# Optimization experiments

Measured on AMD Instinct MI355X. Metric: run time of the kernel, lower is better.

## Reference

```python
import jax, jax.numpy as jnp
import numpy as np
from jax import lax

B, C_IN, C_MID, C_OUT, H, W = 8, 256, 128, 256, 128, 128
DN = ('NCHW', 'OIHW', 'NCHW')


def conv_bn(x, w, scale, shift, pad, relu):
    # conv (bias=False) + eval-mode BatchNorm folded to per-channel scale/shift
    y = lax.conv_general_dilated(x, w, (1, 1), [(pad, pad), (pad, pad)],
                                 dimension_numbers=DN)
    y = y * scale[None, :, None, None] + shift[None, :, None, None]
    return jax.nn.relu(y) if relu else y


def setup_inputs() -> dict:
    key = jax.random.key(0)
    ks = jax.random.split(key, 20)
    d = {"x": jax.random.normal(ks[0], (B, C_IN, H, W), dtype=jnp.float32)}
    f = 0.05  # weight scale
    def wparams(i, cout, cin, k):
        kk = jax.random.split(ks[i], 3)
        return (jax.random.normal(kk[0], (cout, cin, k, k), jnp.float32) * f,
                1.0 + 0.1 * jax.random.normal(kk[1], (cout,), jnp.float32),
                0.1 * jax.random.normal(kk[2], (cout,), jnp.float32))
    d["w_l"], d["s_l"], d["o_l"] = wparams(1, C_MID, C_IN, 3)
    d["w_r"], d["s_r"], d["o_r"] = wparams(2, C_MID, C_IN, 3)
    d["w_t"], d["s_t"], d["o_t"] = wparams(3, C_MID, C_IN, 3)
    d["w_b"], d["s_b"], d["o_b"] = wparams(4, C_MID, C_IN, 3)
    d["w2"], d["s2"], d["o2"] = wparams(5, C_OUT, C_MID, 3)
    d["w1"], d["s1"], d["o1"] = wparams(6, C_IN, C_IN, 1)
    return d


def reference(x, w_l, s_l, o_l, w_r, s_r, o_r, w_t, s_t, o_t,
              w_b, s_b, o_b, w2, s2, o2, w1, s1, o1):
    # four directional branches: conv+bn+relu then corner pooling (cummax scan)
    xl = lax.cummax(conv_bn(x, w_l, s_l, o_l, 1, True), axis=3, reverse=True)  # left: max over w'>=w
    xr = lax.cummax(conv_bn(x, w_r, s_r, o_r, 1, True), axis=3)                # right: max over w'<=w
    xt = lax.cummax(conv_bn(x, w_t, s_t, o_t, 1, True), axis=2, reverse=True)  # top: max over h'>=h
    xb = lax.cummax(conv_bn(x, w_b, s_b, o_b, 1, True), axis=2)                # bottom: max over h'<=h
    x1 = conv_bn(xl + xr + xb + xt, w2, s2, o2, 1, False)  # 3x3 conv+bn, no relu
    x2 = conv_bn(x, w1, s1, o1, 0, False)                  # 1x1 conv+bn skip, no relu
    return jax.nn.relu(x1 + x2)
```

## Files before the change

### kernel.cpp

```cpp
#include <hip/hip_runtime.h>

#define NEG_INF (-3.402823466e+38f)

typedef __bf16 bf16x8 __attribute__((ext_vector_type(8)));
typedef float  f32x16 __attribute__((ext_vector_type(16)));

__device__ __forceinline__ unsigned short f2bf(float f){
    unsigned u = __builtin_bit_cast(unsigned, f);
    u += 0x7fffu + ((u >> 16) & 1u);
    return (unsigned short)(u >> 16);
}
__device__ __forceinline__ float bf2f(unsigned short h){
    unsigned u = ((unsigned)h) << 16;
    return __builtin_bit_cast(float, u);
}

#if defined(__has_builtin)
#if __has_builtin(__builtin_amdgcn_global_load_lds)
#define ASYNC_CP 1
#endif
#endif

__device__ __forceinline__ void gl_lds(const unsigned short* g, unsigned short* lbase, int lane) {
#ifdef ASYNC_CP
    __builtin_amdgcn_global_load_lds(
        (const __attribute__((address_space(1))) unsigned int*)g,
        (__attribute__((address_space(3))) unsigned int*)lbase, 16, 0, 0);
#else
    *(uint4*)(lbase + (size_t)lane * 8) = *(const uint4*)g;
#endif
}

__global__ void __launch_bounds__(256)
k_xpose(const float* __restrict__ x, unsigned short* __restrict__ xh)
{
    __shared__ float tile[64 * 129];
    const int t = threadIdx.x;
    const int ci0 = blockIdx.x * 64, h = blockIdx.y, b = blockIdx.z;
    const float4* src = (const float4*)x;
#pragma unroll
    for (int i = 0; i < 8; ++i) {
        int idx = t + i * 256;
        int ci = idx >> 5, w4 = idx & 31;
        float4 v = src[((b * 256 + ci0 + ci) * 128 + h) * 32 + w4];
        tile[ci * 129 + w4 * 4 + 0] = v.x;
        tile[ci * 129 + w4 * 4 + 1] = v.y;
        tile[ci * 129 + w4 * 4 + 2] = v.z;
        tile[ci * 129 + w4 * 4 + 3] = v.w;
    }
    __syncthreads();
    unsigned* dst = (unsigned*)xh;
#pragma unroll
    for (int i = 0; i < 16; ++i) {
        int idx = t + i * 256;
        int w = idx >> 5, cp = idx & 31;
        float lo = tile[(cp * 2 + 0) * 129 + w];
        float hi = tile[(cp * 2 + 1) * 129 + w];
        dst[((b * 128 + h) * 128 + w) * 128 + (ci0 >> 1) + cp] =
            (unsigned)f2bf(lo) | ((unsigned)f2bf(hi) << 16);
    }
}

__global__ void __launch_bounds__(256)
k_wpack(const float* __restrict__ wl, const float* __restrict__ sl, const float* __restrict__ ol,
        const float* __restrict__ wr, const float* __restrict__ sr, const float* __restrict__ orr,
        const float* __restrict__ wt, const float* __restrict__ st, const float* __restrict__ ot,
        const float* __restrict__ wb, const float* __restrict__ sb, const float* __restrict__ ob,
        const float* __restrict__ w2, const float* __restrict__ s2, const float* __restrict__ o2,
        const float* __restrict__ w1, const float* __restrict__ s1, const float* __restrict__ o1,
        unsigned short* __restrict__ wpkBR, unsigned short* __restrict__ wpk2,
        unsigned short* __restrict__ wpk1, float* __restrict__ shF, float* __restrict__ obF)
{
    int i = blockIdx.x * 256 + threadIdx.x;
    if (i < 1179648) {
        int br = i / 294912, r = i % 294912;
        int c = r / 2304, r2 = r % 2304, ci = r2 / 9, k9 = r2 % 9;
        const float* wp = br == 0 ? wl : br == 1 ? wr : br == 2 ? wt : wb;
        const float* sp = br == 0 ? sl : br == 1 ? sr : br == 2 ? st : sb;
        float v = wp[r] * sp[c];
        int p = (c >> 4) * 64 + br * 16 + (c & 15);
        wpkBR[(((((ci >> 4) * 9 + k9) * 2 + ((ci >> 3) & 1)) * 512 + p) * 8) + (ci & 7)] = f2bf(v);
    } else if (i < 1474560) {
        int j = i - 1179648;
        int c = j / 1152, r2 = j % 1152, ci = r2 / 9, k9 = r2 % 9;
        wpk2[(((((ci >> 4) * 9 + k9) * 2 + ((ci >> 3) & 1)) * 256 + c) * 8) + (ci & 7)] = f2bf(w2[j] * s2[c]);
    } else if (i < 1540096) {
        int j = i - 1474560;
        int c = j >> 8, ci = j & 255;
        wpk1[((((ci >> 4) * 2 + ((ci >> 3) & 1)) * 256 + c) * 8) + (ci & 7)] = f2bf(w1[j] * s1[c]);
    } else if (i < 1540608) {
        int p = i - 1540096;
        int br = (p >> 4) & 3, c = (p >> 6) * 16 + (p & 15);
        const float* op = br == 0 ? ol : br == 1 ? orr : br == 2 ? ot : ob;
        shF[p] = op[c];
    } else if (i < 1540864) {
        int c = i - 1540608;
        obF[c] = o2[c] + o1[c];
    }
}

#define XIN_SH 12672
#define WBUF_SH 9216
__global__ void __launch_bounds__(256, 2)
k_brconv(const unsigned short* __restrict__ xh, const unsigned short* __restrict__ wpkBR,
         const float* __restrict__ shF, unsigned short* __restrict__ sbuf2,
         unsigned short* __restrict__ ytbT, unsigned short* __restrict__ ytbB)
{
    __shared__ __align__(16) unsigned short smem[2 * XIN_SH + WBUF_SH + 128];
    unsigned short* xinA = smem;
    unsigned short* xinB = smem + XIN_SH;
    unsigned short* wbuf = smem + 2 * XIN_SH;
    float* shs = (float*)(smem + 2 * XIN_SH + WBUF_SH);

    const int t = threadIdx.x;
    const int lin = (int)blockIdx.x + ((int)blockIdx.y << 3) + ((int)blockIdx.z << 8);
    const int swz = (lin & 7) * 256 + (lin >> 3);
    const int bx = swz & 7, h0 = ((swz >> 3) & 31) << 2, b = swz >> 8;
    const int wv = t >> 6, lane = t & 63;
    const int lo5 = lane & 31, hi1 = lane >> 5;
    const int hi32 = lane & 32;

    if (t < 64) shs[t] = shF[bx * 64 + t];
    for (int idx = t; idx < 3168; idx += 256)
        *(uint4*)(smem + idx * 8) = make_uint4(0, 0, 0, 0);

    f32x16 acc[2][4];
#pragma unroll
    for (int ct = 0; ct < 2; ++ct)
#pragma unroll
        for (int nb = 0; nb < 4; ++nb)
#pragma unroll
            for (int i = 0; i < 16; ++i) acc[ct][nb][i] = 0.f;

    __syncthreads();

    for (int s = wv; s < 24; s += 4) {
        int r = s >> 2, khi = (s >> 1) & 1, half = s & 1;
        int ih = h0 - 1 + r;
        if (ih >= 0 && ih < 128)
            gl_lds(xh + (((size_t)(b * 128 + ih) * 128 + half * 64 + lane) * 256) + khi * 8,
                   xinA + ((r * 2 + khi) * 132 + 1 + half * 64) * 8, lane);
    }
    for (int s = wv; s < 18; s += 4)
        gl_lds(wpkBR + ((size_t)s * 512 + bx * 64 + lane) * 8, wbuf + s * 512, lane);
    __syncthreads();

    uint4 wr0 = make_uint4(0, 0, 0, 0), wr1 = wr0, wr2 = wr0, wr3 = wr0, wr4 = wr0;
    unsigned short* xcur = xinA;
    unsigned short* xnxt = xinB;

    for (int cb = 0; cb < 16; ++cb) {
        if (cb < 15) {
            const int nc = cb + 1;
            for (int s = wv; s < 24; s += 4) {
                int r = s >> 2, khi = (s >> 1) & 1, half = s & 1;
                int ih = h0 - 1 + r;
                if (ih >= 0 && ih < 128)
                    gl_lds(xh + (((size_t)(b * 128 + ih) * 128 + half * 64 + lane) * 256) + nc * 16 + khi * 8,
                           xnxt + ((r * 2 + khi) * 132 + 1 + half * 64) * 8, lane);
            }
            wr0 = *(const uint4*)(wpkBR + ((size_t)(nc * 18 + wv) * 512 + bx * 64 + lane) * 8);
            wr1 = *(const uint4*)(wpkBR + ((size_t)(nc * 18 + wv + 4) * 512 + bx * 64 + lane) * 8);
            wr2 = *(const uint4*)(wpkBR + ((size_t)(nc * 18 + wv + 8) * 512 + bx * 64 + lane) * 8);
            wr3 = *(const uint4*)(wpkBR + ((size_t)(nc * 18 + wv + 12) * 512 + bx * 64 + lane) * 8);
            if (wv < 2)
                wr4 = *(const uint4*)(wpkBR + ((size_t)(nc * 18 + wv + 16) * 512 + bx * 64 + lane) * 8);
        }
#pragma unroll
        for (int k9 = 0; k9 < 9; ++k9) {
            const int kh = k9 / 3, kw = k9 % 3;
            bf16x8 a0 = *(const bf16x8*)(wbuf + ((k9 * 2 + hi1) * 64 + lo5) * 8);
            bf16x8 a1 = *(const bf16x8*)(wbuf + ((k9 * 2 + hi1) * 64 + 32 + lo5) * 8);
#pragma unroll
            for (int nb = 0; nb < 4; ++nb) {
                bf16x8 bf = *(const bf16x8*)(xcur + (((wv + kh) * 2 + hi1) * 132 + nb * 32 + lo5 + kw) * 8);
                acc[0][nb] = __builtin_amdgcn_mfma_f32_32x32x16_bf16(a0, bf, acc[0][nb], 0, 0, 0);
                acc[1][nb] = __builtin_amdgcn_mfma_f32_32x32x16_bf16(a1, bf, acc[1][nb], 0, 0, 0);
            }
        }
        __syncthreads();
        if (cb < 15) {
            *(uint4*)(wbuf + (wv) * 512 + lane * 8) = wr0;
            *(uint4*)(wbuf + (wv + 4) * 512 + lane * 8) = wr1;
            *(uint4*)(wbuf + (wv + 8) * 512 + lane * 8) = wr2;
            *(uint4*)(wbuf + (wv + 12) * 512 + lane * 8) = wr3;
            if (wv < 2)
                *(uint4*)(wbuf + (wv + 16) * 512 + lane * 8) = wr4;
            __syncthreads();
            unsigned short* tp = xcur; xcur = xnxt; xnxt = tp;
        }
    }

    unsigned short* pbw = smem + wv * 3072;
    const int hg = h0 + wv;

#pragma unroll
    for (int r = 0; r < 8; ++r) {
        const int m = (r & 3) + 8 * (r >> 2) + 4 * hi1;
        const float shv = shs[m];
        float carry = NEG_INF;
#pragma unroll
        for (int nn = 3; nn >= 0; --nn) {
            float a = fmaxf(acc[0][nn][r] + shv, 0.f);
#pragma unroll
            for (int d = 1; d < 32; d <<= 1) {
                float o = __shfl_down(a, d);
                if (lo5 < 32 - d) a = fmaxf(a, o);
            }
            a = fmaxf(a, carry);
            carry = __shfl(a, hi32);
            acc[0][nn][r] = a;
        }
    }
#pragma unroll
    for (int r = 8; r < 16; ++r) {
        const int m = 16 + (r & 3) + 8 * ((r >> 2) & 1) + 4 * hi1;
        const float shv = shs[m];
        float carry = NEG_INF;
#pragma unroll
        for (int nn = 0; nn < 4; ++nn) {
            float a = fmaxf(acc[0][nn][r] + shv, 0.f);
#pragma unroll
            for (int d = 1; d < 32; d <<= 1) {
                float o = __shfl_up(a, d);
                if (lo5 >= d) a = fmaxf(a, o);
            }
            a = fmaxf(a, carry);
            carry = __shfl(a, hi32 | 31);
            acc[0][nn][r] = a;
        }
    }
#pragma unroll
    for (int r = 0; r < 8; ++r) {
        const int c16 = (r & 3) + 8 * (r >> 2) + 4 * hi1;
#pragma unroll
        for (int nn = 0; nn < 4; ++nn)
            pbw[(nn * 32 + lo5) * 24 + c16] = f2bf(acc[0][nn][r] + acc[0][nn][r + 8]);
    }
    {
        unsigned short* gdst = sbuf2 + ((size_t)(b * 128 + hg) * 128) * 128 + bx * 16;
#pragma unroll
        for (int i = 0; i < 4; ++i) {
            int idx = lane + i * 64;
            int w = idx >> 1, part = idx & 1;
            *(uint4*)(gdst + (size_t)w * 128 + part * 8) = *(const uint4*)(pbw + w * 24 + part * 8);
        }
    }
#pragma unroll
    for (int r = 0; r < 8; ++r) {
        const int c16 = (r & 3) + 8 * (r >> 2) + 4 * hi1;
        const float shv = shs[32 + c16];
#pragma unroll
        for (int nn = 0; nn < 4; ++nn)
            pbw[(nn * 32 + lo5) * 24 + c16] = f2bf(fmaxf(acc[1][nn][r] + shv, 0.f));
    }
    {
        unsigned short* gdst = ytbT + ((size_t)(b * 128 + hg) * 128) * 128 + bx * 16;
#pragma unroll
        for (int i = 0; i < 4; ++i) {
            int idx = lane + i * 64;
            int w = idx >> 1, part = idx & 1;
            *(uint4*)(gdst + (size_t)w * 128 + part * 8) = *(const uint4*)(pbw + w * 24 + part * 8);
        }
    }
#pragma unroll
    for (int r = 8; r < 16; ++r) {
        const int c16 = (r & 3) + 8 * ((r >> 2) & 1) + 4 * hi1;
        const float shv = shs[48 + c16];
#pragma unroll
        for (int nn = 0; nn < 4; ++nn)
            pbw[(nn * 32 + lo5) * 24 + c16] = f2bf(fmaxf(acc[1][nn][r] + shv, 0.f));
    }
    {
        unsigned short* gdst = ytbB + ((size_t)(b * 128 + hg) * 128) * 128 + bx * 16;
#pragma unroll
        for (int i = 0; i < 4; ++i) {
            int idx = lane + i * 64;
            int w = idx >> 1, part = idx & 1;
            *(uint4*)(gdst + (size_t)w * 128 + part * 8) = *(const uint4*)(pbw + w * 24 + part * 8);
        }
    }
}

__global__ void __launch_bounds__(256)
k_colscan2(const unsigned short* __restrict__ ytbT, const unsigned short* __restrict__ ytbB,
           unsigned short* __restrict__ sbuf2)
{
    __shared__ float tile[8][8][33];
    const int t = threadIdx.x;
    const int w0 = blockIdx.x * 8, c0 = blockIdx.y * 32, b = blockIdx.z;
    const int sc = t & 31, sw = t >> 5;
    const int rh = t >> 5, r5 = t & 31;
    const int rw = r5 >> 2, rcq = r5 & 3;

    {
        float cum = NEG_INF;
        for (int step = 0; step < 16; ++step) {
            int h0 = 120 - step * 8;
            for (int q = 0; q < 8; ++q) {
                int hh = 7 - q;
                int hg = h0 + hh;
                float v = bf2f(ytbT[((b * 128 + hg) * 128 + (w0 + sw)) * 128 + c0 + sc]);
                cum = fmaxf(cum, v);
                tile[hh][sw][sc] = cum;
            }
            __syncthreads();
            {
                int hg = h0 + rh;
                unsigned short* p = sbuf2 + ((b * 128 + hg) * 128 + w0 + rw) * 128 + c0 + rcq * 8;
                uint4 u = *(uint4*)p;
                unsigned short* us = (unsigned short*)&u;
#pragma unroll
                for (int j = 0; j < 8; ++j)
                    us[j] = f2bf(bf2f(us[j]) + tile[rh][rw][rcq * 8 + j]);
                *(uint4*)p = u;
            }
            __syncthreads();
        }
    }
    {
        float cum = NEG_INF;
        for (int step = 0; step < 16; ++step) {
            int h0 = step * 8;
            for (int q = 0; q < 8; ++q) {
                int hh = q;
                int hg = h0 + hh;
                float v = bf2f(ytbB[((b * 128 + hg) * 128 + (w0 + sw)) * 128 + c0 + sc]);
                cum = fmaxf(cum, v);
                tile[hh][sw][sc] = cum;
            }
            __syncthreads();
            {
                int hg = h0 + rh;
                unsigned short* p = sbuf2 + ((b * 128 + hg) * 128 + w0 + rw) * 128 + c0 + rcq * 8;
                uint4 u = *(uint4*)p;
                unsigned short* us = (unsigned short*)&u;
#pragma unroll
                for (int j = 0; j < 8; ++j)
                    us[j] = f2bf(bf2f(us[j]) + tile[rh][rw][rcq * 8 + j]);
                *(uint4*)p = u;
            }
            __syncthreads();
        }
    }
}

__global__ void __launch_bounds__(256, 2)
k_final(const unsigned short* __restrict__ sbuf2, const unsigned short* __restrict__ xh,
        const unsigned short* __restrict__ wpk2, const unsigned short* __restrict__ wpk1,
        const float* __restrict__ obF, float* __restrict__ out)
{
    __shared__ __align__(16) unsigned short smem[2 * XIN_SH + WBUF_SH + 128];
    unsigned short* xinA = smem;
    unsigned short* xinB = smem + XIN_SH;
    unsigned short* wbuf = smem + 2 * XIN_SH;
    float* obs = (float*)(smem + 2 * XIN_SH + WBUF_SH);

    const int t = threadIdx.x;
    const int lin = (int)blockIdx.x + ((int)blockIdx.y << 2) + ((int)blockIdx.z << 7);
    const int swz = (lin & 7) * 128 + (lin >> 3);
    const int bx = swz & 3, h0 = ((swz >> 2) & 31) << 2, b = swz >> 7;
    const int wv = t >> 6, lane = t & 63;
    const int lo5 = lane & 31, hi1 = lane >> 5;

    if (t < 64) obs[t] = obF[bx * 64 + t];
    for (int idx = t; idx < 3168; idx += 256)
        *(uint4*)(smem + idx * 8) = make_uint4(0, 0, 0, 0);

    f32x16 acc[2][4];
#pragma unroll
    for (int ct = 0; ct < 2; ++ct)
#pragma unroll
        for (int nb = 0; nb < 4; ++nb)
#pragma unroll
            for (int i = 0; i < 16; ++i) acc[ct][nb][i] = 0.f;

    __syncthreads();

    for (int s = wv; s < 24; s += 4) {
        int r = s >> 2, khi = (s >> 1) & 1, half = s & 1;
        int ih = h0 - 1 + r;
        if (ih >= 0 && ih < 128)
            gl_lds(sbuf2 + (((size_t)(b * 128 + ih) * 128 + half * 64 + lane) * 128) + khi * 8,
                   xinA + ((r * 2 + khi) * 132 + 1 + half * 64) * 8, lane);
    }
    for (int s = wv; s < 18; s += 4)
        gl_lds(wpk2 + ((size_t)s * 256 + bx * 64 + lane) * 8, wbuf + s * 512, lane);
    __syncthreads();

    uint4 wr0 = make_uint4(0, 0, 0, 0), wr1 = wr0, wr2 = wr0, wr3 = wr0, wr4 = wr0;
    unsigned short* xcur = xinA;
    unsigned short* xnxt = xinB;

    for (int cb = 0; cb < 8; ++cb) {
        if (cb < 7) {
            const int nc = cb + 1;
            for (int s = wv; s < 24; s += 4) {
                int r = s >> 2, khi = (s >> 1) & 1, half = s & 1;
                int ih = h0 - 1 + r;
                if (ih >= 0 && ih < 128)
                    gl_lds(sbuf2 + (((size_t)(b * 128 + ih) * 128 + half * 64 + lane) * 128) + nc * 16 + khi * 8,
                           xnxt + ((r * 2 + khi) * 132 + 1 + half * 64) * 8, lane);
            }
            wr0 = *(const uint4*)(wpk2 + ((size_t)(nc * 18 + wv) * 256 + bx * 64 + lane) * 8);
            wr1 = *(const uint4*)(wpk2 + ((size_t)(nc * 18 + wv + 4) * 256 + bx * 64 + lane) * 8);
            wr2 = *(const uint4*)(wpk2 + ((size_t)(nc * 18 + wv + 8) * 256 + bx * 64 + lane) * 8);
            wr3 = *(const uint4*)(wpk2 + ((size_t)(nc * 18 + wv + 12) * 256 + bx * 64 + lane) * 8);
            if (wv < 2)
                wr4 = *(const uint4*)(wpk2 + ((size_t)(nc * 18 + wv + 16) * 256 + bx * 64 + lane) * 8);
        }
#pragma unroll
        for (int k9 = 0; k9 < 9; ++k9) {
            const int kh = k9 / 3, kw = k9 % 3;
            bf16x8 a0 = *(const bf16x8*)(wbuf + ((k9 * 2 + hi1) * 64 + lo5) * 8);
            bf16x8 a1 = *(const bf16x8*)(wbuf + ((k9 * 2 + hi1) * 64 + 32 + lo5) * 8);
#pragma unroll
            for (int nb = 0; nb < 4; ++nb) {
                bf16x8 bf = *(const bf16x8*)(xcur + (((wv + kh) * 2 + hi1) * 132 + nb * 32 + lo5 + kw) * 8);
                acc[0][nb] = __builtin_amdgcn_mfma_f32_32x32x16_bf16(a0, bf, acc[0][nb], 0, 0, 0);
                acc[1][nb] = __builtin_amdgcn_mfma_f32_32x32x16_bf16(a1, bf, acc[1][nb], 0, 0, 0);
            }
        }
        __syncthreads();
        if (cb < 7) {
            *(uint4*)(wbuf + (wv) * 512 + lane * 8) = wr0;
            *(uint4*)(wbuf + (wv + 4) * 512 + lane * 8) = wr1;
            *(uint4*)(wbuf + (wv + 8) * 512 + lane * 8) = wr2;
            *(uint4*)(wbuf + (wv + 12) * 512 + lane * 8) = wr3;
            if (wv < 2)
                *(uint4*)(wbuf + (wv + 16) * 512 + lane * 8) = wr4;
            __syncthreads();
            unsigned short* tp = xcur; xcur = xnxt; xnxt = tp;
        }
    }

    {
        const unsigned short* xrow = xh + ((size_t)(b * 128 + h0 + wv) * 128) * 256 + hi1 * 8;
        const unsigned short* w1p  = wpk1 + ((size_t)hi1 * 256 + bx * 64) * 8;
#pragma unroll 4
        for (int cb = 0; cb < 16; ++cb) {
            bf16x8 a0 = *(const bf16x8*)(w1p + ((size_t)cb * 512 + lo5) * 8);
            bf16x8 a1 = *(const bf16x8*)(w1p + ((size_t)cb * 512 + 32 + lo5) * 8);
#pragma unroll
            for (int nb = 0; nb < 4; ++nb) {
                bf16x8 bf = *(const bf16x8*)(xrow + (size_t)(nb * 32 + lo5) * 256 + cb * 16);
                acc[0][nb] = __builtin_amdgcn_mfma_f32_32x32x16_bf16(a0, bf, acc[0][nb], 0, 0, 0);
                acc[1][nb] = __builtin_amdgcn_mfma_f32_32x32x16_bf16(a1, bf, acc[1][nb], 0, 0, 0);
            }
        }
    }

    const int hg = h0 + wv;
#pragma unroll
    for (int ct = 0; ct < 2; ++ct)
#pragma unroll
        for (int r = 0; r < 16; ++r) {
            const int m = ct * 32 + (r & 3) + 8 * (r >> 2) + 4 * hi1;
            const float bias = obs[m];
#pragma unroll
            for (int nb = 0; nb < 4; ++nb)
                out[((size_t)(b * 256 + bx * 64 + m) * 128 + hg) * 128 + nb * 32 + lo5] =
                    fmaxf(acc[ct][nb][r] + bias, 0.f);
        }
}

extern "C" void kernel_launch(void* const* d_in, const int* in_sizes, int n_in,
                              void* d_out, int out_size, void* d_ws, size_t ws_size,
                              hipStream_t stream)
{
    const float* x   = (const float*)d_in[0];
    const float* w_l = (const float*)d_in[1];
    const float* s_l = (const float*)d_in[2];
    const float* o_l = (const float*)d_in[3];
    const float* w_r = (const float*)d_in[4];
    const float* s_r = (const float*)d_in[5];
    const float* o_r = (const float*)d_in[6];
    const float* w_t = (const float*)d_in[7];
    const float* s_t = (const float*)d_in[8];
    const float* o_t = (const float*)d_in[9];
    const float* w_b = (const float*)d_in[10];
    const float* s_b = (const float*)d_in[11];
    const float* o_b = (const float*)d_in[12];
    const float* w2  = (const float*)d_in[13];
    const float* s2  = (const float*)d_in[14];
    const float* o2  = (const float*)d_in[15];
    const float* w1  = (const float*)d_in[16];
    const float* s1  = (const float*)d_in[17];
    const float* o1  = (const float*)d_in[18];
    float* out = (float*)d_out;
    char*  ws  = (char*)d_ws;

    unsigned short* xh    = (unsigned short*)(ws + 0);
    unsigned short* sbuf2 = (unsigned short*)(ws + 67108864);
    unsigned short* wpkBR = (unsigned short*)(ws + 100663296);
    unsigned short* wpk2  = (unsigned short*)(ws + 103022592);
    unsigned short* wpk1  = (unsigned short*)(ws + 103612416);
    float* shF = (float*)(ws + 103743488);
    float* obF = (float*)(ws + 103745536);

    unsigned short* ytbT = (unsigned short*)d_out;
    unsigned short* ytbB = ytbT + 16777216;

    dim3 blk(256);
    k_xpose<<<dim3(4, 128, 8), blk, 0, stream>>>(x, xh);
    k_wpack<<<dim3(6019), blk, 0, stream>>>(w_l, s_l, o_l, w_r, s_r, o_r,
                                            w_t, s_t, o_t, w_b, s_b, o_b,
                                            w2, s2, o2, w1, s1, o1,
                                            wpkBR, wpk2, wpk1, shF, obF);
    k_brconv<<<dim3(8, 32, 8), blk, 0, stream>>>(xh, wpkBR, shF, sbuf2, ytbT, ytbB);
    k_colscan2<<<dim3(16, 4, 8), blk, 0, stream>>>(ytbT, ytbB, sbuf2);
    k_final<<<dim3(4, 32, 8), blk, 0, stream>>>(sbuf2, xh, wpk2, wpk1, obF, out);
}
```

Before: 681.3 us.

## Rewrite column cummax scan as per-thread register scan; raise MFMA wave priority

The column-scan kernel drops its shared-memory tile and barriers. Each thread now owns 8 contiguous channels at one (b,w) and walks all 128 rows sequentially, keeping the running max in registers and using 16-byte vector loads and stores. The grid shrinks from 512 blocks to 64, so far fewer waves are available to hide memory latency on a long serial dependence chain. Separately, s_setprio brackets the MFMA inner loops in both conv kernels to favor waves issuing matrix work.

```diff
diff --git a/kernel.cpp b/kernel.cpp
--- a/kernel.cpp
+++ b/kernel.cpp
@@ -166,6 +166,7 @@
             if (wv < 2)
                 wr4 = *(const uint4*)(wpkBR + ((size_t)(nc * 18 + wv + 16) * 512 + bx * 64 + lane) * 8);
         }
+        __builtin_amdgcn_s_setprio(1);
 #pragma unroll
         for (int k9 = 0; k9 < 9; ++k9) {
             const int kh = k9 / 3, kw = k9 % 3;
@@ -178,6 +179,7 @@
                 acc[1][nb] = __builtin_amdgcn_mfma_f32_32x32x16_bf16(a1, bf, acc[1][nb], 0, 0, 0);
             }
         }
+        __builtin_amdgcn_s_setprio(0);
         __syncthreads();
         if (cb < 15) {
             *(uint4*)(wbuf + (wv) * 512 + lane * 8) = wr0;
@@ -286,61 +288,46 @@
 k_colscan2(const unsigned short* __restrict__ ytbT, const unsigned short* __restrict__ ytbB,
            unsigned short* __restrict__ sbuf2)
 {
-    __shared__ float tile[8][8][33];
     const int t = threadIdx.x;
-    const int w0 = blockIdx.x * 8, c0 = blockIdx.y * 32, b = blockIdx.z;
-    const int sc = t & 31, sw = t >> 5;
-    const int rh = t >> 5, r5 = t & 31;
-    const int rw = r5 >> 2, rcq = r5 & 3;
+    const int b = blockIdx.x, wx = blockIdx.y;
+    const int w = wx * 16 + (t >> 4), cp = (t & 15) * 8;
+    const size_t hs = 128 * 128;
+    const size_t base = ((size_t)(b * 128) * 128 + w) * 128 + cp;
 
     {
-        float cum = NEG_INF;
-        for (int step = 0; step < 16; ++step) {
-            int h0 = 120 - step * 8;
-            for (int q = 0; q < 8; ++q) {
-                int hh = 7 - q;
-                int hg = h0 + hh;
-                float v = bf2f(ytbT[((b * 128 + hg) * 128 + (w0 + sw)) * 128 + c0 + sc]);
-                cum = fmaxf(cum, v);
-                tile[hh][sw][sc] = cum;
-            }
-            __syncthreads();
-            {
-                int hg = h0 + rh;
-                unsigned short* p = sbuf2 + ((b * 128 + hg) * 128 + w0 + rw) * 128 + c0 + rcq * 8;
-                uint4 u = *(uint4*)p;
-                unsigned short* us = (unsigned short*)&u;
-#pragma unroll
-                for (int j = 0; j < 8; ++j)
-                    us[j] = f2bf(bf2f(us[j]) + tile[rh][rw][rcq * 8 + j]);
-                *(uint4*)p = u;
-            }
-            __syncthreads();
+        float cum[8];
+#pragma unroll
+        for (int j = 0; j < 8; ++j) cum[j] = NEG_INF;
+#pragma unroll 8
+        for (int h = 127; h >= 0; --h) {
+            uint4 tv = *(const uint4*)(ytbT + base + (size_t)h * hs);
+            uint4 sv = *(uint4*)(sbuf2 + base + (size_t)h * hs);
+            unsigned short* tp = (unsigned short*)&tv;
+            unsigned short* sp = (unsigned short*)&sv;
+#pragma unroll
+            for (int j = 0; j < 8; ++j) {
+                cum[j] = fmaxf(cum[j], bf2f(tp[j]));
+                sp[j] = f2bf(bf2f(sp[j]) + cum[j]);
+            }
+            *(uint4*)(sbuf2 + base + (size_t)h * hs) = sv;
         }
     }
     {
-        float cum = NEG_INF;
-        for (int step = 0; step < 16; ++step) {
-            int h0 = step * 8;
-            for (int q = 0; q < 8; ++q) {
-                int hh = q;
-                int hg = h0 + hh;
-                float v = bf2f(ytbB[((b * 128 + hg) * 128 + (w0 + sw)) * 128 + c0 + sc]);
-                cum = fmaxf(cum, v);
-                tile[hh][sw][sc] = cum;
-            }
-            __syncthreads();
-            {
-                int hg = h0 + rh;
-                unsigned short* p = sbuf2 + ((b * 128 + hg) * 128 + w0 + rw) * 128 + c0 + rcq * 8;
-                uint4 u = *(uint4*)p;
-                unsigned short* us = (unsigned short*)&u;
-#pragma unroll
-                for (int j = 0; j < 8; ++j)
-                    us[j] = f2bf(bf2f(us[j]) + tile[rh][rw][rcq * 8 + j]);
-                *(uint4*)p = u;
-            }
-            __syncthreads();
+        float cum[8];
+#pragma unroll
+        for (int j = 0; j < 8; ++j) cum[j] = NEG_INF;
+#pragma unroll 8
+        for (int h = 0; h < 128; ++h) {
+            uint4 tv = *(const uint4*)(ytbB + base + (size_t)h * hs);
+            uint4 sv = *(uint4*)(sbuf2 + base + (size_t)h * hs);
+            unsigned short* tp = (unsigned short*)&tv;
+            unsigned short* sp = (unsigned short*)&sv;
+#pragma unroll
+            for (int j = 0; j < 8; ++j) {
+                cum[j] = fmaxf(cum[j], bf2f(tp[j]));
+                sp[j] = f2bf(bf2f(sp[j]) + cum[j]);
+            }
+            *(uint4*)(sbuf2 + base + (size_t)h * hs) = sv;
         }
     }
 }
@@ -409,6 +396,7 @@
             if (wv < 2)
                 wr4 = *(const uint4*)(wpk2 + ((size_t)(nc * 18 + wv + 16) * 256 + bx * 64 + lane) * 8);
         }
+        __builtin_amdgcn_s_setprio(1);
 #pragma unroll
         for (int k9 = 0; k9 < 9; ++k9) {
             const int kh = k9 / 3, kw = k9 % 3;
@@ -421,6 +409,7 @@
                 acc[1][nb] = __builtin_amdgcn_mfma_f32_32x32x16_bf16(a1, bf, acc[1][nb], 0, 0, 0);
             }
         }
+        __builtin_amdgcn_s_setprio(0);
         __syncthreads();
         if (cb < 7) {
             *(uint4*)(wbuf + (wv) * 512 + lane * 8) = wr0;
@@ -508,6 +497,6 @@
                                             w2, s2, o2, w1, s1, o1,
                                             wpkBR, wpk2, wpk1, shF, obF);
     k_brconv<<<dim3(8, 32, 8), blk, 0, stream>>>(xh, wpkBR, shF, sbuf2, ytbT, ytbB);
-    k_colscan2<<<dim3(16, 4, 8), blk, 0, stream>>>(ytbT, ytbB, sbuf2);
+    k_colscan2<<<dim3(8, 8), blk, 0, stream>>>(ytbT, ytbB, sbuf2);
     k_final<<<dim3(4, 32, 8), blk, 0, stream>>>(sbuf2, xh, wpk2, wpk1, obF, out);
 }
```

After: 816.8 us. +19.9%, slower.
